# Kernel optimization log

Hardware: AMD Instinct MI355X
Metric: run time of the kernel (lower is better)

The kernel has to match this reference:

```python
import jax, jax.numpy as jnp
import numpy as np

HIDDEN = 1024
HEADS = 16
HEAD_DIM = HIDDEN // HEADS
B, S = 2, 2048
LN_EPS = 1e-5


def setup_inputs() -> dict:
    key = jax.random.key(0)
    ks = jax.random.split(key, 5)
    sc = 0.02
    return {
        "hidden_states": jax.random.normal(ks[0], (B, S, HIDDEN), dtype=jnp.float32),
        "w_qkv": jax.random.normal(ks[1], (HIDDEN, 3 * HIDDEN), dtype=jnp.float32) * sc,
        "b_qkv": jax.random.normal(ks[2], (3 * HIDDEN,), dtype=jnp.float32) * sc,
        "w_dense": jax.random.normal(ks[3], (HIDDEN, HIDDEN), dtype=jnp.float32) * sc,
        "b_dense": jax.random.normal(ks[4], (HIDDEN,), dtype=jnp.float32) * sc,
        "ln_gamma": jnp.ones((HIDDEN,), dtype=jnp.float32),
        "ln_beta": jnp.zeros((HIDDEN,), dtype=jnp.float32),
    }


def reference(hidden_states, w_qkv, b_qkv, w_dense, b_dense, ln_gamma, ln_beta):
    b, s, h = hidden_states.shape
    head_dim = h // HEADS
    # fused QKV projection: [B,S,3H] -> [B,S,heads,3*head_dim] -> [B,heads,S,3*head_dim]
    qkv = hidden_states @ w_qkv + b_qkv
    qkv = qkv.reshape(b, s, HEADS, 3 * head_dim).transpose(0, 2, 1, 3)
    q, k, v = jnp.split(qkv, 3, axis=-1)  # each [B,heads,S,head_dim]
    # scaled dot-product attention (no mask in the non-fused path of the original)
    scores = jnp.einsum("bhqd,bhkd->bhqk", q, k) / jnp.sqrt(jnp.float32(head_dim))
    probs = jax.nn.softmax(scores, axis=-1)
    ctx = jnp.einsum("bhqk,bhkd->bhqd", probs, v)
    ctx = ctx.transpose(0, 2, 1, 3).reshape(b, s, h)  # [B,S,H]
    # output projection + residual + LayerNorm
    out = ctx @ w_dense + b_dense
    x = out + hidden_states
    mu = jnp.mean(x, axis=-1, keepdims=True)
    var = jnp.mean(jnp.square(x - mu), axis=-1, keepdims=True)
    return (x - mu) * jax.lax.rsqrt(var + LN_EPS) * ln_gamma + ln_beta
```

## Files before the change

kernel.cpp:

```cpp
#include <hip/hip_runtime.h>
#include <hip/hip_bf16.h>

#define HIDDEN 1024
#define SEQ 2048
#define NH 16

typedef float f32x4 __attribute__((ext_vector_type(4)));
typedef __bf16 bf16x8 __attribute__((ext_vector_type(8)));
typedef short s16x4 __attribute__((ext_vector_type(4)));
typedef short s16x8 __attribute__((ext_vector_type(8)));

typedef __attribute__((address_space(1))) unsigned int gu32;
typedef __attribute__((address_space(3))) unsigned int lu32;

__device__ __forceinline__ unsigned short f2bf(float f) {
  union { float f; unsigned u; } v; v.f = f;
  unsigned u = v.u;
  u = (u + 0x7fffu + ((u >> 16) & 1u)) >> 16;
  return (unsigned short)u;
}

__device__ __forceinline__ float bf2f(unsigned short u) {
  union { unsigned v; float f; } t; t.v = (unsigned)u << 16; return t.f;
}

__device__ __forceinline__ void gload16(const unsigned short* g, unsigned short* l) {
  __builtin_amdgcn_global_load_lds((gu32*)(void*)g, (lu32*)(void*)l, 16, 0, 0);
}

__device__ __forceinline__ f32x4 mfma32(bf16x8 a, bf16x8 b, f32x4 c) {
  return __builtin_amdgcn_mfma_f32_16x16x32_bf16(a, b, c, 0, 0, 0);
}
__device__ __forceinline__ f32x4 mfma16(s16x4 a, s16x4 b, f32x4 c) {
  return __builtin_amdgcn_mfma_f32_16x16x16bf16_1k(a, b, c, 0, 0, 0);
}

__device__ __forceinline__ unsigned sch(float s) {
  return (unsigned)(int)fmaf(s, 128.0f, 16250.99f);
}

__global__ __launch_bounds__(256) void k_cast(const float* __restrict__ x,
                                              unsigned short* __restrict__ y, int n4) {
  int i = blockIdx.x * 256 + threadIdx.x;
  if (i < n4) {
    float4 v = ((const float4*)x)[i];
    ushort4 r;
    r.x = f2bf(v.x); r.y = f2bf(v.y); r.z = f2bf(v.z); r.w = f2bf(v.w);
    ((ushort4*)y)[i] = r;
  }
}

__global__ __launch_bounds__(256) void k_transpose(const float* __restrict__ W,
                                                   unsigned short* __restrict__ Wt,
                                                   int K, int N) {
  __shared__ unsigned short t[32][33];
  int n0 = blockIdx.x * 32, k0 = blockIdx.y * 32;
  int tx = threadIdx.x & 31, ty = threadIdx.x >> 5;
  #pragma unroll
  for (int i = ty; i < 32; i += 8)
    t[i][tx] = f2bf(W[(size_t)(k0 + i) * N + n0 + tx]);
  __syncthreads();
  #pragma unroll
  for (int i = ty; i < 32; i += 8)
    Wt[(size_t)(n0 + i) * K + k0 + tx] = t[tx][i];
}

__global__ __launch_bounds__(256) void k_gemm_qkv(
    const unsigned short* __restrict__ A, const unsigned short* __restrict__ Bt,
    const float* __restrict__ bias, unsigned short* __restrict__ Qg,
    unsigned short* __restrict__ Kg, unsigned short* __restrict__ Vg) {
  __shared__ unsigned short As[128 * 32];
  __shared__ unsigned short Bs[128 * 32];
  const int K = 1024;
  const int tid = threadIdx.x;
  const int lane = tid & 63;
  const int wave = tid >> 6;
  const int wm = wave >> 1, wn = wave & 1;
  const int quad = lane >> 4, l16 = lane & 15;
  const int srow = lane >> 2, scol = (lane & 3) << 3;
  const int bm = blockIdx.y * 128, bn = blockIdx.x * 128;

  f32x4 acc[4][4] = {};

  const unsigned short* gA = A + (size_t)(bm + wave * 16 + srow) * K + scol;
  const unsigned short* gA2 = gA + (size_t)64 * K;
  const unsigned short* gB = Bt + (size_t)(bn + wave * 16 + srow) * K + scol;
  const unsigned short* gB2 = gB + (size_t)64 * K;
  unsigned short* lA = &As[wave * 512];
  unsigned short* lA2 = &As[(wave + 4) * 512];
  unsigned short* lB = &Bs[wave * 512];
  unsigned short* lB2 = &Bs[(wave + 4) * 512];

  for (int k0 = 0; k0 < K; k0 += 32) {
    gload16(gA + k0, lA);
    gload16(gA2 + k0, lA2);
    gload16(gB + k0, lB);
    gload16(gB2 + k0, lB2);
    __syncthreads();
    bf16x8 af[4], bfr[4];
    #pragma unroll
    for (int i = 0; i < 4; i++)
      af[i] = *(const bf16x8*)&As[(wm * 64 + i * 16 + l16) * 32 + quad * 8];
    #pragma unroll
    for (int i = 0; i < 4; i++)
      bfr[i] = *(const bf16x8*)&Bs[(wn * 64 + i * 16 + l16) * 32 + quad * 8];
    #pragma unroll
    for (int mi = 0; mi < 4; mi++)
      #pragma unroll
      for (int ni = 0; ni < 4; ni++)
        acc[mi][ni] = mfma32(af[mi], bfr[ni], acc[mi][ni]);
    __syncthreads();
  }

  const int b = bm >> 11;
  const int qb = bm & 2047;
  const float c2 = 0.18033688011112042f;
  #pragma unroll
  for (int ni = 0; ni < 4; ni++) {
    const int cs = bn + wn * 64 + ni * 16;
    const int head = cs / 192;
    const int which = (cs % 192) >> 6;
    const int d = (cs & 63) + l16;
    const int bh = b * 16 + head;
    const float bv = bias[cs + l16];
    #pragma unroll
    for (int mi = 0; mi < 4; mi++) {
      const int q0r = qb + wm * 64 + mi * 16 + quad * 4;
      if (which == 0) {
        #pragma unroll
        for (int r = 0; r < 4; r++)
          Qg[((size_t)bh * SEQ + q0r + r) * 64 + d] =
              f2bf((acc[mi][ni][r] + bv) * c2);
      } else if (which == 1) {
        #pragma unroll
        for (int r = 0; r < 4; r++)
          Kg[((size_t)bh * SEQ + q0r + r) * 64 + d] = f2bf(acc[mi][ni][r] + bv);
      } else {
        ushort4 pk;
        pk.x = f2bf(acc[mi][ni][0] + bv);
        pk.y = f2bf(acc[mi][ni][1] + bv);
        pk.z = f2bf(acc[mi][ni][2] + bv);
        pk.w = f2bf(acc[mi][ni][3] + bv);
        *(ushort4*)&Vg[((size_t)bh * 64 + d) * SEQ + (q0r >> 6) * 64 +
                       16 * quad + 4 * mi] = pk;
      }
    }
  }
}

__global__ __launch_bounds__(256, 4) void k_attn(const unsigned short* __restrict__ Qg,
                                                 const unsigned short* __restrict__ Kg,
                                                 const unsigned short* __restrict__ Vg,
                                                 unsigned short* __restrict__ Op,
                                                 float* __restrict__ Lp) {
  __shared__ unsigned short Ks[2][64 * 32];
  __shared__ unsigned short Vs[64 * 88];
  const int tid = threadIdx.x, lane = tid & 63, wave = tid >> 6;
  const int quad = lane >> 4, l16 = lane & 15;
  const int srow = lane >> 2, scol = (lane & 3) << 3;
  const int bh = blockIdx.y;
  const int z = blockIdx.z;
  const int q0 = blockIdx.x * 128 + wave * 32;

  bf16x8 Qf[2][2];
  #pragma unroll
  for (int qt = 0; qt < 2; qt++)
    #pragma unroll
    for (int kh = 0; kh < 2; kh++)
      Qf[qt][kh] = *(const bf16x8*)(Qg + ((size_t)bh * SEQ + q0 + qt * 16 + l16) * 64 +
                                    kh * 32 + quad * 8);

  f32x4 o[2][4] = {};
  f32x4 ol[2] = {};
  const s16x4 ones = {16256, 16256, 16256, 16256};

  const int vrow = wave * 16 + (lane >> 3);
  const int vcol = (lane & 7) << 3;

  for (int kt = z * 16; kt < z * 16 + 16; kt++) {
    const int k0 = kt * 64;
    const unsigned short* gK = Kg + ((size_t)bh * SEQ + k0 + wave * 16 + srow) * 64 + scol;
    gload16(gK, &Ks[0][wave * 512]);
    gload16(gK + 32, &Ks[1][wave * 512]);
    const unsigned short* gV = Vg + ((size_t)bh * 64 + vrow) * SEQ + k0 + vcol;
    uint4 v0 = *(const uint4*)gV;
    uint4 v1 = *(const uint4*)(gV + 8 * SEQ);
    *(uint4*)&Vs[vrow * 88 + vcol] = v0;
    *(uint4*)&Vs[(vrow + 8) * 88 + vcol] = v1;
    __syncthreads();

    bf16x8 Af[4][2];
    #pragma unroll
    for (int nt = 0; nt < 4; nt++) {
      Af[nt][0] = *(const bf16x8*)&Ks[0][(nt * 16 + l16) * 32 + quad * 8];
      Af[nt][1] = *(const bf16x8*)&Ks[1][(nt * 16 + l16) * 32 + quad * 8];
    }
    s16x4 Pf[2][4];
    #pragma unroll
    for (int qt = 0; qt < 2; qt++)
      #pragma unroll
      for (int nt = 0; nt < 4; nt++) {
        f32x4 s = {0.f, 0.f, 0.f, 0.f};
        s = mfma32(Af[nt][0], Qf[qt][0], s);
        s = mfma32(Af[nt][1], Qf[qt][1], s);
        union { unsigned u[2]; s16x4 v; } pu;
        unsigned u0 = sch(s[0]), u1 = sch(s[1]);
        unsigned u2 = sch(s[2]), u3 = sch(s[3]);
        pu.u[0] = __builtin_amdgcn_perm(u1, u0, 0x05040100u);
        pu.u[1] = __builtin_amdgcn_perm(u3, u2, 0x05040100u);
        Pf[qt][nt] = pu.v;
      }
    #pragma unroll
    for (int nd = 0; nd < 4; nd++) {
      s16x8 vv0 = *(const s16x8*)&Vs[(nd * 16 + l16) * 88 + quad * 16];
      s16x8 vv1 = *(const s16x8*)&Vs[(nd * 16 + l16) * 88 + quad * 16 + 8];
      s16x4 vf[4];
      vf[0] = __builtin_shufflevector(vv0, vv0, 0, 1, 2, 3);
      vf[1] = __builtin_shufflevector(vv0, vv0, 4, 5, 6, 7);
      vf[2] = __builtin_shufflevector(vv1, vv1, 0, 1, 2, 3);
      vf[3] = __builtin_shufflevector(vv1, vv1, 4, 5, 6, 7);
      #pragma unroll
      for (int nt = 0; nt < 4; nt++) {
        o[0][nd] = mfma16(Pf[0][nt], vf[nt], o[0][nd]);
        o[1][nd] = mfma16(Pf[1][nt], vf[nt], o[1][nd]);
      }
    }
    #pragma unroll
    for (int nt = 0; nt < 4; nt++) {
      ol[0] = mfma16(Pf[0][nt], ones, ol[0]);
      ol[1] = mfma16(Pf[1][nt], ones, ol[1]);
    }
    __syncthreads();
  }

  const size_t obase = (size_t)z * 4194304 + (size_t)bh * SEQ * 64;
  #pragma unroll
  for (int qt = 0; qt < 2; qt++) {
    #pragma unroll
    for (int r = 0; r < 4; r++) {
      int q = q0 + qt * 16 + quad * 4 + r;
      #pragma unroll
      for (int nd = 0; nd < 4; nd++)
        Op[obase + (size_t)q * 64 + nd * 16 + l16] = f2bf(o[qt][nd][r]);
      if (l16 == 0) Lp[z * 65536 + bh * SEQ + q] = ol[qt][r];
    }
  }
}

__global__ __launch_bounds__(256) void k_combine(const unsigned short* __restrict__ Op,
                                                 const float* __restrict__ Lp,
                                                 unsigned short* __restrict__ ctx) {
  int gid = blockIdx.x * 256 + threadIdx.x;
  int bh = gid >> 15, rem = gid & 32767;
  int q = rem >> 4, d0 = (rem & 15) << 2;
  float il = 1.0f / (Lp[bh * SEQ + q] + Lp[65536 + bh * SEQ + q]);
  size_t o0 = ((size_t)bh * SEQ + q) * 64 + d0;
  ushort4 a = *(const ushort4*)(Op + o0);
  ushort4 c = *(const ushort4*)(Op + 4194304 + o0);
  ushort4 r;
  r.x = f2bf((bf2f(a.x) + bf2f(c.x)) * il);
  r.y = f2bf((bf2f(a.y) + bf2f(c.y)) * il);
  r.z = f2bf((bf2f(a.z) + bf2f(c.z)) * il);
  r.w = f2bf((bf2f(a.w) + bf2f(c.w)) * il);
  int b = bh >> 4, h = bh & 15;
  *(ushort4*)(ctx + ((size_t)b * SEQ + q) * HIDDEN + h * 64 + d0) = r;
}

__global__ __launch_bounds__(256) void k_gemm_dense(
    const unsigned short* __restrict__ A, const unsigned short* __restrict__ Bt,
    const float* __restrict__ bias, const float* __restrict__ res,
    float* __restrict__ Cf) {
  __shared__ unsigned short As[64 * 32];
  __shared__ unsigned short Bs[64 * 32];
  const int K = 1024, N = 1024;
  const int tid = threadIdx.x, lane = tid & 63, wave = tid >> 6;
  const int wm = wave >> 1, wn = wave & 1;
  const int quad = lane >> 4, l16 = lane & 15;
  const int bm = blockIdx.y * 64, bn = blockIdx.x * 64;

  f32x4 acc[2][2] = {};
  const unsigned short* gA = A + (size_t)(bm + (tid >> 2)) * K + ((tid & 3) << 3);
  const unsigned short* gB = Bt + (size_t)(bn + (tid >> 2)) * K + ((tid & 3) << 3);
  unsigned short* lA = &As[wave * 512];
  unsigned short* lB = &Bs[wave * 512];

  for (int k0 = 0; k0 < K; k0 += 32) {
    gload16(gA + k0, lA);
    gload16(gB + k0, lB);
    __syncthreads();
    bf16x8 af[2], bfr[2];
    #pragma unroll
    for (int i = 0; i < 2; i++)
      af[i] = *(const bf16x8*)&As[(wm * 32 + i * 16 + l16) * 32 + quad * 8];
    #pragma unroll
    for (int i = 0; i < 2; i++)
      bfr[i] = *(const bf16x8*)&Bs[(wn * 32 + i * 16 + l16) * 32 + quad * 8];
    #pragma unroll
    for (int mi = 0; mi < 2; mi++)
      #pragma unroll
      for (int ni = 0; ni < 2; ni++)
        acc[mi][ni] = mfma32(af[mi], bfr[ni], acc[mi][ni]);
    __syncthreads();
  }

  #pragma unroll
  for (int mi = 0; mi < 2; mi++)
    #pragma unroll
    for (int ni = 0; ni < 2; ni++) {
      int col = bn + wn * 32 + ni * 16 + l16;
      float bv = bias[col];
      #pragma unroll
      for (int r = 0; r < 4; r++) {
        int row = bm + wm * 32 + mi * 16 + quad * 4 + r;
        Cf[(size_t)row * N + col] = acc[mi][ni][r] + bv + res[(size_t)row * N + col];
      }
    }
}

__global__ __launch_bounds__(256) void k_ln(const float* __restrict__ x,
                                            const float* __restrict__ g,
                                            const float* __restrict__ be,
                                            float* __restrict__ out) {
  __shared__ float red[8];
  const int row = blockIdx.x, tid = threadIdx.x;
  const float* xr = x + (size_t)row * HIDDEN;
  float4 v = ((const float4*)xr)[tid];
  float s = v.x + v.y + v.z + v.w;
  float s2 = v.x * v.x + v.y * v.y + v.z * v.z + v.w * v.w;
  #pragma unroll
  for (int off = 32; off >= 1; off >>= 1) {
    s += __shfl_xor(s, off, 64);
    s2 += __shfl_xor(s2, off, 64);
  }
  const int wave = tid >> 6, lane = tid & 63;
  if (lane == 0) { red[wave * 2] = s; red[wave * 2 + 1] = s2; }
  __syncthreads();
  float ts = red[0] + red[2] + red[4] + red[6];
  float ts2 = red[1] + red[3] + red[5] + red[7];
  float mu = ts * (1.f / HIDDEN);
  float var = ts2 * (1.f / HIDDEN) - mu * mu;
  float rs = rsqrtf(var + 1e-5f);
  float4 gv = ((const float4*)g)[tid];
  float4 bv = ((const float4*)be)[tid];
  float4 o;
  o.x = (v.x - mu) * rs * gv.x + bv.x;
  o.y = (v.y - mu) * rs * gv.y + bv.y;
  o.z = (v.z - mu) * rs * gv.z + bv.z;
  o.w = (v.w - mu) * rs * gv.w + bv.w;
  ((float4*)(out + (size_t)row * HIDDEN))[tid] = o;
}

extern "C" void kernel_launch(void* const* d_in, const int* in_sizes, int n_in,
                              void* d_out, int out_size, void* d_ws, size_t ws_size,
                              hipStream_t stream) {
  const float* hs      = (const float*)d_in[0];
  const float* w_qkv   = (const float*)d_in[1];
  const float* b_qkv   = (const float*)d_in[2];
  const float* w_dense = (const float*)d_in[3];
  const float* b_dense = (const float*)d_in[4];
  const float* ln_g    = (const float*)d_in[5];
  const float* ln_b    = (const float*)d_in[6];
  float* out = (float*)d_out;

  char* ws = (char*)d_ws;
  unsigned short* Xb  = (unsigned short*)(ws + 0);
  unsigned short* Op  = (unsigned short*)(ws + 0);
  unsigned short* Wqt = (unsigned short*)(ws + 8388608);
  unsigned short* Qg  = (unsigned short*)(ws + 16777216);
  float* Xr           = (float*)(ws + 16777216);
  unsigned short* Kg  = (unsigned short*)(ws + 25165824);
  unsigned short* Vg  = (unsigned short*)(ws + 33554432);
  unsigned short* Ctx = (unsigned short*)(ws + 41943040);
  float* Lp           = (float*)(ws + 50331648);
  unsigned short* Wdt = (unsigned short*)(ws + 50855936);

  k_cast<<<4096, 256, 0, stream>>>(hs, Xb, 1048576);
  k_transpose<<<dim3(96, 32), 256, 0, stream>>>(w_qkv, Wqt, 1024, 3072);
  k_transpose<<<dim3(32, 32), 256, 0, stream>>>(w_dense, Wdt, 1024, 1024);
  k_gemm_qkv<<<dim3(24, 32), 256, 0, stream>>>(Xb, Wqt, b_qkv, Qg, Kg, Vg);
  k_attn<<<dim3(16, 32, 2), 256, 0, stream>>>(Qg, Kg, Vg, Op, Lp);
  k_combine<<<4096, 256, 0, stream>>>(Op, Lp, Ctx);
  k_gemm_dense<<<dim3(16, 64), 256, 0, stream>>>(Ctx, Wdt, b_dense, hs, Xr);
  k_ln<<<4096, 256, 0, stream>>>(Xr, ln_g, ln_b, out);
}
```

Before: 220.4 us.

## Merge prep kernels, deepen GEMM K-steps to 64, vectorize V stores

The cast kernel and the two weight-transpose kernels become a single launch that dispatches on block index, removing two kernel launches. Both GEMMs now load two 32-wide K slabs per barrier pair, halving the number of __syncthreads in the main loop at the cost of twice the LDS per block. The QKV GEMM also gets an occupancy hint in its launch bounds, and its V-transpose epilogue writes 16 contiguous bf16 values with two 16-byte stores instead of four 8-byte stores.

```diff
diff --git a/kernel.cpp b/kernel.cpp
--- a/kernel.cpp
+++ b/kernel.cpp
@@ -39,22 +39,33 @@
   return (unsigned)(int)fmaf(s, 128.0f, 16250.99f);
 }
 
-__global__ __launch_bounds__(256) void k_cast(const float* __restrict__ x,
-                                              unsigned short* __restrict__ y, int n4) {
-  int i = blockIdx.x * 256 + threadIdx.x;
-  if (i < n4) {
-    float4 v = ((const float4*)x)[i];
+__global__ __launch_bounds__(256) void k_prep(const float* __restrict__ hs,
+                                              unsigned short* __restrict__ Xb,
+                                              const float* __restrict__ w_qkv,
+                                              unsigned short* __restrict__ Wqt,
+                                              const float* __restrict__ w_dense,
+                                              unsigned short* __restrict__ Wdt) {
+  __shared__ unsigned short t[32][33];
+  const int bid = blockIdx.x;
+  if (bid < 4096) {
+    int i = bid * 256 + threadIdx.x;
+    float4 v = ((const float4*)hs)[i];
     ushort4 r;
     r.x = f2bf(v.x); r.y = f2bf(v.y); r.z = f2bf(v.z); r.w = f2bf(v.w);
-    ((ushort4*)y)[i] = r;
-  }
-}
-
-__global__ __launch_bounds__(256) void k_transpose(const float* __restrict__ W,
-                                                   unsigned short* __restrict__ Wt,
-                                                   int K, int N) {
-  __shared__ unsigned short t[32][33];
-  int n0 = blockIdx.x * 32, k0 = blockIdx.y * 32;
+    ((ushort4*)Xb)[i] = r;
+    return;
+  }
+  const float* W; unsigned short* Wt; int N, n0, k0;
+  if (bid < 4096 + 3072) {
+    int b2 = bid - 4096;
+    W = w_qkv; Wt = Wqt; N = 3072;
+    n0 = (b2 % 96) * 32; k0 = (b2 / 96) * 32;
+  } else {
+    int b3 = bid - 7168;
+    W = w_dense; Wt = Wdt; N = 1024;
+    n0 = (b3 % 32) * 32; k0 = (b3 / 32) * 32;
+  }
+  const int K = 1024;
   int tx = threadIdx.x & 31, ty = threadIdx.x >> 5;
   #pragma unroll
   for (int i = ty; i < 32; i += 8)
@@ -65,12 +76,12 @@
     Wt[(size_t)(n0 + i) * K + k0 + tx] = t[tx][i];
 }
 
-__global__ __launch_bounds__(256) void k_gemm_qkv(
+__global__ __launch_bounds__(256, 4) void k_gemm_qkv(
     const unsigned short* __restrict__ A, const unsigned short* __restrict__ Bt,
     const float* __restrict__ bias, unsigned short* __restrict__ Qg,
     unsigned short* __restrict__ Kg, unsigned short* __restrict__ Vg) {
-  __shared__ unsigned short As[128 * 32];
-  __shared__ unsigned short Bs[128 * 32];
+  __shared__ unsigned short As0[128 * 32], As1[128 * 32];
+  __shared__ unsigned short Bs0[128 * 32], Bs1[128 * 32];
   const int K = 1024;
   const int tid = threadIdx.x;
   const int lane = tid & 63;
@@ -86,29 +97,42 @@
   const unsigned short* gA2 = gA + (size_t)64 * K;
   const unsigned short* gB = Bt + (size_t)(bn + wave * 16 + srow) * K + scol;
   const unsigned short* gB2 = gB + (size_t)64 * K;
-  unsigned short* lA = &As[wave * 512];
-  unsigned short* lA2 = &As[(wave + 4) * 512];
-  unsigned short* lB = &Bs[wave * 512];
-  unsigned short* lB2 = &Bs[(wave + 4) * 512];
-
-  for (int k0 = 0; k0 < K; k0 += 32) {
-    gload16(gA + k0, lA);
-    gload16(gA2 + k0, lA2);
-    gload16(gB + k0, lB);
-    gload16(gB2 + k0, lB2);
-    __syncthreads();
-    bf16x8 af[4], bfr[4];
-    #pragma unroll
-    for (int i = 0; i < 4; i++)
-      af[i] = *(const bf16x8*)&As[(wm * 64 + i * 16 + l16) * 32 + quad * 8];
-    #pragma unroll
-    for (int i = 0; i < 4; i++)
-      bfr[i] = *(const bf16x8*)&Bs[(wn * 64 + i * 16 + l16) * 32 + quad * 8];
-    #pragma unroll
-    for (int mi = 0; mi < 4; mi++)
-      #pragma unroll
-      for (int ni = 0; ni < 4; ni++)
-        acc[mi][ni] = mfma32(af[mi], bfr[ni], acc[mi][ni]);
+  unsigned short* lA0 = &As0[wave * 512];
+  unsigned short* lA0b = &As0[(wave + 4) * 512];
+  unsigned short* lA1 = &As1[wave * 512];
+  unsigned short* lA1b = &As1[(wave + 4) * 512];
+  unsigned short* lB0 = &Bs0[wave * 512];
+  unsigned short* lB0b = &Bs0[(wave + 4) * 512];
+  unsigned short* lB1 = &Bs1[wave * 512];
+  unsigned short* lB1b = &Bs1[(wave + 4) * 512];
+
+  for (int k0 = 0; k0 < K; k0 += 64) {
+    gload16(gA + k0, lA0);
+    gload16(gA2 + k0, lA0b);
+    gload16(gA + k0 + 32, lA1);
+    gload16(gA2 + k0 + 32, lA1b);
+    gload16(gB + k0, lB0);
+    gload16(gB2 + k0, lB0b);
+    gload16(gB + k0 + 32, lB1);
+    gload16(gB2 + k0 + 32, lB1b);
+    __syncthreads();
+    #pragma unroll
+    for (int ph = 0; ph < 2; ph++) {
+      const unsigned short* Ap = ph ? As1 : As0;
+      const unsigned short* Bp = ph ? Bs1 : Bs0;
+      bf16x8 af[4], bfr[4];
+      #pragma unroll
+      for (int i = 0; i < 4; i++)
+        af[i] = *(const bf16x8*)&Ap[(wm * 64 + i * 16 + l16) * 32 + quad * 8];
+      #pragma unroll
+      for (int i = 0; i < 4; i++)
+        bfr[i] = *(const bf16x8*)&Bp[(wn * 64 + i * 16 + l16) * 32 + quad * 8];
+      #pragma unroll
+      for (int mi = 0; mi < 4; mi++)
+        #pragma unroll
+        for (int ni = 0; ni < 4; ni++)
+          acc[mi][ni] = mfma32(af[mi], bfr[ni], acc[mi][ni]);
+    }
     __syncthreads();
   }
 
@@ -123,26 +147,33 @@
     const int d = (cs & 63) + l16;
     const int bh = b * 16 + head;
     const float bv = bias[cs + l16];
-    #pragma unroll
-    for (int mi = 0; mi < 4; mi++) {
-      const int q0r = qb + wm * 64 + mi * 16 + quad * 4;
-      if (which == 0) {
+    if (which == 2) {
+      unsigned short pk[16];
+      #pragma unroll
+      for (int mi = 0; mi < 4; mi++)
+        #pragma unroll
+        for (int r = 0; r < 4; r++)
+          pk[mi * 4 + r] = f2bf(acc[mi][ni][r] + bv);
+      const int kb = (qb + wm * 64) >> 6;
+      unsigned short* vp = &Vg[((size_t)bh * 64 + d) * SEQ + kb * 64 + 16 * quad];
+      *(uint4*)vp = *(const uint4*)&pk[0];
+      *(uint4*)(vp + 8) = *(const uint4*)&pk[8];
+    } else if (which == 0) {
+      #pragma unroll
+      for (int mi = 0; mi < 4; mi++) {
+        const int q0r = qb + wm * 64 + mi * 16 + quad * 4;
         #pragma unroll
         for (int r = 0; r < 4; r++)
           Qg[((size_t)bh * SEQ + q0r + r) * 64 + d] =
               f2bf((acc[mi][ni][r] + bv) * c2);
-      } else if (which == 1) {
+      }
+    } else {
+      #pragma unroll
+      for (int mi = 0; mi < 4; mi++) {
+        const int q0r = qb + wm * 64 + mi * 16 + quad * 4;
         #pragma unroll
         for (int r = 0; r < 4; r++)
           Kg[((size_t)bh * SEQ + q0r + r) * 64 + d] = f2bf(acc[mi][ni][r] + bv);
-      } else {
-        ushort4 pk;
-        pk.x = f2bf(acc[mi][ni][0] + bv);
-        pk.y = f2bf(acc[mi][ni][1] + bv);
-        pk.z = f2bf(acc[mi][ni][2] + bv);
-        pk.w = f2bf(acc[mi][ni][3] + bv);
-        *(ushort4*)&Vg[((size_t)bh * 64 + d) * SEQ + (q0r >> 6) * 64 +
-                       16 * quad + 4 * mi] = pk;
       }
     }
   }
@@ -270,8 +301,8 @@
     const unsigned short* __restrict__ A, const unsigned short* __restrict__ Bt,
     const float* __restrict__ bias, const float* __restrict__ res,
     float* __restrict__ Cf) {
-  __shared__ unsigned short As[64 * 32];
-  __shared__ unsigned short Bs[64 * 32];
+  __shared__ unsigned short As0[64 * 32], As1[64 * 32];
+  __shared__ unsigned short Bs0[64 * 32], Bs1[64 * 32];
   const int K = 1024, N = 1024;
   const int tid = threadIdx.x, lane = tid & 63, wave = tid >> 6;
   const int wm = wave >> 1, wn = wave & 1;
@@ -281,25 +312,34 @@
   f32x4 acc[2][2] = {};
   const unsigned short* gA = A + (size_t)(bm + (tid >> 2)) * K + ((tid & 3) << 3);
   const unsigned short* gB = Bt + (size_t)(bn + (tid >> 2)) * K + ((tid & 3) << 3);
-  unsigned short* lA = &As[wave * 512];
-  unsigned short* lB = &Bs[wave * 512];
-
-  for (int k0 = 0; k0 < K; k0 += 32) {
-    gload16(gA + k0, lA);
-    gload16(gB + k0, lB);
-    __syncthreads();
-    bf16x8 af[2], bfr[2];
-    #pragma unroll
-    for (int i = 0; i < 2; i++)
-      af[i] = *(const bf16x8*)&As[(wm * 32 + i * 16 + l16) * 32 + quad * 8];
-    #pragma unroll
-    for (int i = 0; i < 2; i++)
-      bfr[i] = *(const bf16x8*)&Bs[(wn * 32 + i * 16 + l16) * 32 + quad * 8];
-    #pragma unroll
-    for (int mi = 0; mi < 2; mi++)
-      #pragma unroll
-      for (int ni = 0; ni < 2; ni++)
-        acc[mi][ni] = mfma32(af[mi], bfr[ni], acc[mi][ni]);
+  unsigned short* lA0 = &As0[wave * 512];
+  unsigned short* lA1 = &As1[wave * 512];
+  unsigned short* lB0 = &Bs0[wave * 512];
+  unsigned short* lB1 = &Bs1[wave * 512];
+
+  for (int k0 = 0; k0 < K; k0 += 64) {
+    gload16(gA + k0, lA0);
+    gload16(gA + k0 + 32, lA1);
+    gload16(gB + k0, lB0);
+    gload16(gB + k0 + 32, lB1);
+    __syncthreads();
+    #pragma unroll
+    for (int ph = 0; ph < 2; ph++) {
+      const unsigned short* Ap = ph ? As1 : As0;
+      const unsigned short* Bp = ph ? Bs1 : Bs0;
+      bf16x8 af[2], bfr[2];
+      #pragma unroll
+      for (int i = 0; i < 2; i++)
+        af[i] = *(const bf16x8*)&Ap[(wm * 32 + i * 16 + l16) * 32 + quad * 8];
+      #pragma unroll
+      for (int i = 0; i < 2; i++)
+        bfr[i] = *(const bf16x8*)&Bp[(wn * 32 + i * 16 + l16) * 32 + quad * 8];
+      #pragma unroll
+      for (int mi = 0; mi < 2; mi++)
+        #pragma unroll
+        for (int ni = 0; ni < 2; ni++)
+          acc[mi][ni] = mfma32(af[mi], bfr[ni], acc[mi][ni]);
+    }
     __syncthreads();
   }
 
@@ -374,9 +414,7 @@
   float* Lp           = (float*)(ws + 50331648);
   unsigned short* Wdt = (unsigned short*)(ws + 50855936);
 
-  k_cast<<<4096, 256, 0, stream>>>(hs, Xb, 1048576);
-  k_transpose<<<dim3(96, 32), 256, 0, stream>>>(w_qkv, Wqt, 1024, 3072);
-  k_transpose<<<dim3(32, 32), 256, 0, stream>>>(w_dense, Wdt, 1024, 1024);
+  k_prep<<<8192, 256, 0, stream>>>(hs, Xb, w_qkv, Wqt, w_dense, Wdt);
   k_gemm_qkv<<<dim3(24, 32), 256, 0, stream>>>(Xb, Wqt, b_qkv, Qg, Kg, Vg);
   k_attn<<<dim3(16, 32, 2), 256, 0, stream>>>(Qg, Kg, Vg, Op, Lp);
   k_combine<<<4096, 256, 0, stream>>>(Op, Lp, Ctx);
```

New measurement: 200.7 us. 1.1x faster.
